# Performance work log

Hardware: AMD Instinct MI355X
Metric: run time of the kernel (lower is better)

The kernel has to match this reference:

```python
import jax, jax.numpy as jnp
import numpy as np


def median_filter(image, kernel_size):
    """kxk sliding-window median with reflect padding, same spatial size.
    image: [B, C, H, W] float. kernel_size: odd Python int."""
    k = int(kernel_size)
    p = k // 2
    B, C, H, W = image.shape
    xp = jnp.pad(image, ((0, 0), (0, 0), (p, p), (p, p)), mode='reflect')
    # k*k shifted views stacked on a new last axis: [B, C, H, W, k*k]
    windows = jnp.stack(
        [xp[:, :, i:i + H, j:j + W] for i in range(k) for j in range(k)],
        axis=-1,
    )
    # k odd -> k*k odd -> exact middle element (matches torch.median selection)
    return jnp.median(windows, axis=-1)


def setup_inputs() -> dict:
    key = jax.random.key(0)
    k1, _ = jax.random.split(key)
    image = jax.random.uniform(k1, (8, 3, 512, 512), dtype=jnp.float32)
    mask = jnp.ones((8, 1, 512, 512), dtype=jnp.float32)
    return {"image": image, "mask": mask, "kernel_size": 5}


def reference(image, mask, kernel_size):
    med = median_filter(image, kernel_size)
    # passthrough=True: (median - image).detach() + image
    out = image + jax.lax.stop_gradient(med - image)
    return (out, mask)
```

## Files before the change

kernel.cpp:

```cpp
#include <hip/hip_runtime.h>
#include <cstddef>
#include <cstdint>


#define OTW 64
#define OTH 32

using u32 = uint32_t;

__device__ __forceinline__ u32 pmin(u32 a, u32 b) {
    u32 r;
    asm("v_pk_min_f16 %0, %1, %2" : "=v"(r) : "v"(a), "v"(b));
    return r;
}
__device__ __forceinline__ u32 pmax(u32 a, u32 b) {
    u32 r;
    asm("v_pk_max_f16 %0, %1, %2" : "=v"(r) : "v"(a), "v"(b));
    return r;
}
__device__ __forceinline__ void cep(u32& a, u32& b) {
    u32 lo = pmin(a, b);
    u32 hi = pmax(a, b);
    a = lo;
    b = hi;
}

typedef __fp16 h2_t __attribute__((ext_vector_type(2)));

__device__ __forceinline__ u32 pkrtz(float a, float b) {
    h2_t v = __builtin_amdgcn_cvt_pkrtz(a, b);
    u32 u;
    __builtin_memcpy(&u, &v, 4);
    return u;
}
__device__ __forceinline__ float lo16(u32 v) {
    unsigned short s = (unsigned short)(v & 0xffffu);
    __fp16 h;
    __builtin_memcpy(&h, &s, 2);
    return (float)h;
}
__device__ __forceinline__ float hi16(u32 v) {
    unsigned short s = (unsigned short)(v >> 16);
    __fp16 h;
    __builtin_memcpy(&h, &s, 2);
    return (float)h;
}

__device__ __forceinline__ void sort5p(u32 x[5]) {
    cep(x[0], x[1]); cep(x[3], x[4]); cep(x[2], x[4]); cep(x[2], x[3]);
    cep(x[0], x[3]); cep(x[0], x[2]); cep(x[1], x[4]); cep(x[1], x[3]);
    cep(x[1], x[2]);
}

__device__ __forceinline__ void oem22p(u32 x0, u32 x1, u32 y0, u32 y1,
                                       u32 z[4]) {
    u32 d0 = pmin(x0, y0), d1 = pmax(x0, y0);
    u32 e0 = pmin(x1, y1), e1 = pmax(x1, y1);
    z[0] = d0;
    z[1] = pmin(d1, e0);
    z[2] = pmax(d1, e0);
    z[3] = e1;
}

__device__ __forceinline__ void oem33p(u32 x0, u32 x1, u32 x2, u32 y0, u32 y1,
                                       u32 y2, u32 z[6]) {
    u32 d[4];
    oem22p(x0, x2, y0, y2, d);
    u32 e0 = pmin(x1, y1);
    u32 e1 = pmax(x1, y1);
    z[0] = d[0];
    z[1] = pmin(d[1], e0); z[2] = pmax(d[1], e0);
    z[3] = pmin(d[2], e1); z[4] = pmax(d[2], e1);
    z[5] = d[3];
}

__device__ __forceinline__ void oem55p(const u32 x[5], const u32 y[5],
                                       u32 z[10]) {
    u32 d[6];
    oem33p(x[0], x[2], x[4], y[0], y[2], y[4], d);
    u32 e[4];
    oem22p(x[1], x[3], y[1], y[3], e);
    z[0] = d[0];
    z[1] = pmin(d[1], e[0]); z[2] = pmax(d[1], e[0]);
    z[3] = pmin(d[2], e[1]); z[4] = pmax(d[2], e[1]);
    z[5] = pmin(d[3], e[2]); z[6] = pmax(d[3], e[2]);
    z[7] = pmin(d[4], e[3]); z[8] = pmax(d[4], e[3]);
    z[9] = d[5];
}

__device__ __forceinline__ void oem1010_mid_p(const u32 a[10], const u32 b[10],
                                              u32 u[6]) {
    u32 ae[5] = {a[0], a[2], a[4], a[6], a[8]};
    u32 be[5] = {b[0], b[2], b[4], b[6], b[8]};
    u32 ao[5] = {a[1], a[3], a[5], a[7], a[9]};
    u32 bo[5] = {b[1], b[3], b[5], b[7], b[9]};
    u32 d[10], e[10];
    oem55p(ae, be, d);
    oem55p(ao, bo, e);
    u[0] = pmin(d[4], e[3]); u[1] = pmax(d[4], e[3]);
    u[2] = pmin(d[5], e[4]); u[3] = pmax(d[5], e[4]);
    u[4] = pmin(d[6], e[5]); u[5] = pmax(d[6], e[5]);
}

__device__ __forceinline__ u32 oem65_z5_p(const u32 u[6], const u32 v[5]) {
    u32 d[6];
    oem33p(u[0], u[2], u[4], v[0], v[2], v[4], d);
    u32 dp1 = pmax(u[1], v[1]);
    u32 t1 = pmin(dp1, u[5]);
    u32 e2 = pmax(t1, pmin(u[3], v[3]));
    return pmin(d[3], e2);
}

__device__ __forceinline__ void medrow_p(const u32 c[8][5], u32 med4[4]) {
    u32 M12[10], M34[10], M56[10];
    oem55p(c[1], c[2], M12);
    oem55p(c[3], c[4], M34);
    u32 u[6];
    oem1010_mid_p(M12, M34, u);
    med4[0] = oem65_z5_p(u, c[0]);
    med4[1] = oem65_z5_p(u, c[5]);
    oem55p(c[5], c[6], M56);
    oem1010_mid_p(M34, M56, u);
    med4[2] = oem65_z5_p(u, c[2]);
    med4[3] = oem65_z5_p(u, c[7]);
}

__device__ __forceinline__ int reflect_idx(int i, int n) {
    i = i < 0 ? -i : i;
    i = i >= n ? 2 * n - 2 - i : i;
    return i;
}

__global__ __launch_bounds__(256) void median5_kernel(
    const float* __restrict__ img, const float* __restrict__ mask,
    float* __restrict__ out, const int* __restrict__ kptr, int H, int W,
    int nimg, long img_total) {
    const int tx = threadIdx.x;
    const int ty = threadIdx.y;
    const int x0 = blockIdx.x * OTW;
    const int y0 = blockIdx.y * OTH;
    const int z = blockIdx.z;

    if (z >= nimg) {
        const size_t base = (size_t)(z - nimg) * H * W;
        const int ox = x0 + 4 * tx;
        const int oy = y0 + 2 * ty;
        const float* ms = mask + base + (size_t)oy * W + ox;
        float* md = out + img_total + base + (size_t)oy * W + ox;
        *reinterpret_cast<float4*>(md) = *reinterpret_cast<const float4*>(ms);
        *reinterpret_cast<float4*>(md + W) =
            *reinterpret_cast<const float4*>(ms + W);
        return;
    }
    if (*kptr != 5) return;

    __shared__ float tile[OTH + 4][OTW + 4 + 1];

    const float* __restrict__ src = img + (size_t)z * H * W;
    const int tid = ty * 16 + tx;

    const int NEL = (OTH + 4) * (OTW + 4);
#pragma unroll
    for (int s = 0; s < 10; ++s) {
        int idx = tid + s * 256;
        if (idx < NEL) {
            int r = idx / (OTW + 4);
            int c = idx - r * (OTW + 4);
            int gy = reflect_idx(y0 - 2 + r, H);
            int gx = reflect_idx(x0 - 2 + c, W);
            tile[r][c] = src[(size_t)gy * W + gx];
        }
    }
    __syncthreads();

    float c[8][6];
#pragma unroll
    for (int r = 0; r < 6; ++r) {
#pragma unroll
        for (int j = 0; j < 8; j += 2) {
            float2 v =
                *reinterpret_cast<const float2*>(&tile[2 * ty + r][4 * tx + j]);
            c[j][r] = v.x;
            c[j + 1][r] = v.y;
        }
    }

    u32 P[8][5];
#pragma unroll
    for (int j = 0; j < 8; ++j) {
#pragma unroll
        for (int i = 0; i < 5; ++i) P[j][i] = pkrtz(c[j][i], c[j][i + 1]);
        sort5p(P[j]);
    }

    u32 medp[4];
    medrow_p(P, medp);

    const int ox = x0 + 4 * tx;
    const int oyA = y0 + 2 * ty;
    float* dst = out + (size_t)z * H * W + (size_t)oyA * W + ox;
    *reinterpret_cast<float4*>(dst) =
        make_float4(lo16(medp[0]), lo16(medp[1]), lo16(medp[2]), lo16(medp[3]));
    *reinterpret_cast<float4*>(dst + W) =
        make_float4(hi16(medp[0]), hi16(medp[1]), hi16(medp[2]), hi16(medp[3]));
}

#define MAXK 7
__global__ void median_generic_kernel(const float* __restrict__ img,
                                      float* __restrict__ out,
                                      const int* __restrict__ kptr, int H,
                                      int W, long total) {
    const int k = *kptr;
    if (k == 5 || k > MAXK || (k & 1) == 0 || k < 1) return;
    const long stride = (long)gridDim.x * blockDim.x;
    long i0 = (long)blockIdx.x * blockDim.x + threadIdx.x;
    if (k == 1) {
        for (long i = i0; i < total; i += stride) out[i] = img[i];
        return;
    }
    const int p = k / 2;
    const int n = k * k;
    const int m = n / 2;
    float win[MAXK * MAXK];
    for (long i = i0; i < total; i += stride) {
        int x = (int)(i % W);
        long t = i / W;
        int y = (int)(t % H);
        long img_id = t / H;
        const float* src = img + img_id * (long)H * W;
        int cnt = 0;
        for (int dy = -p; dy <= p; ++dy) {
            int gy = reflect_idx(y + dy, H);
            for (int dx = -p; dx <= p; ++dx) {
                int gx = reflect_idx(x + dx, W);
                win[cnt++] = src[(long)gy * W + gx];
            }
        }
        for (int a = 0; a <= m; ++a) {
            int mi = a;
            for (int b = a + 1; b < n; ++b)
                if (win[b] < win[mi]) mi = b;
            float tv = win[a];
            win[a] = win[mi];
            win[mi] = tv;
        }
        out[i] = win[m];
    }
}

extern "C" void kernel_launch(void* const* d_in, const int* in_sizes, int n_in,
                              void* d_out, int out_size, void* d_ws,
                              size_t ws_size, hipStream_t stream) {
    const float* img = (const float*)d_in[0];
    const float* mask = (const float*)d_in[1];
    const int* kptr = (const int*)d_in[2];
    float* out = (float*)d_out;

    const int H = 512, W = 512;
    const long img_elems = in_sizes[0];
    const long mask_elems = in_sizes[1];
    const int nimg = (int)(img_elems / ((long)H * W));
    const int nmask = (int)(mask_elems / ((long)H * W));

    dim3 block(16, 16);
    dim3 grid(W / OTW, H / OTH, nimg + nmask);
    median5_kernel<<<grid, block, 0, stream>>>(img, mask, out, kptr, H, W,
                                               nimg, img_elems);

    median_generic_kernel<<<512, 256, 0, stream>>>(img, out, kptr, H, W,
                                                   img_elems);
}
```

Baseline: 28.29 us.

## Vectorize halo tile loads and fold generic median path into main kernel

The shared-memory tile load changes from scalar per-element loads with division and double reflection to float4 row loads for the interior, plus a small scalar pass that writes the four halo columns into extra slots at the end of each row. The read-back indexes those relocated halo columns for edge threads. The separate generic-k kernel launch is removed and its work moved into a noinline device function called from the main kernel, which saves one kernel launch per call. The cost is more complex indexing and a 68-wide tile without padding, which may bring back LDS bank conflicts.

```diff
diff --git a/kernel.cpp b/kernel.cpp
--- a/kernel.cpp
+++ b/kernel.cpp
@@ -131,6 +131,48 @@
     return i;
 }
 
+#define MAXK 7
+__device__ __noinline__ void generic_path(const float* __restrict__ src,
+                                          float* __restrict__ dst, int k,
+                                          int H, int W, int ox, int oy) {
+    if (k < 1 || k > MAXK || (k & 1) == 0) return;
+    if (k == 1) {
+#pragma unroll
+        for (int yy = 0; yy < 2; ++yy)
+#pragma unroll
+            for (int xx = 0; xx < 4; ++xx)
+                dst[(size_t)(oy + yy) * W + ox + xx] =
+                    src[(size_t)(oy + yy) * W + ox + xx];
+        return;
+    }
+    const int p = k / 2;
+    const int n = k * k;
+    const int m = n / 2;
+    float win[MAXK * MAXK];
+    for (int yy = 0; yy < 2; ++yy) {
+        for (int xx = 0; xx < 4; ++xx) {
+            int x = ox + xx, y = oy + yy;
+            int cnt = 0;
+            for (int dy = -p; dy <= p; ++dy) {
+                int gy = reflect_idx(y + dy, H);
+                for (int dx = -p; dx <= p; ++dx) {
+                    int gx = reflect_idx(x + dx, W);
+                    win[cnt++] = src[(size_t)gy * W + gx];
+                }
+            }
+            for (int a = 0; a <= m; ++a) {
+                int mi = a;
+                for (int b = a + 1; b < n; ++b)
+                    if (win[b] < win[mi]) mi = b;
+                float tv = win[a];
+                win[a] = win[mi];
+                win[mi] = tv;
+            }
+            dst[(size_t)y * W + x] = win[m];
+        }
+    }
+}
+
 __global__ __launch_bounds__(256) void median5_kernel(
     const float* __restrict__ img, const float* __restrict__ mask,
     float* __restrict__ out, const int* __restrict__ kptr, int H, int W,
@@ -152,37 +194,60 @@
             *reinterpret_cast<const float4*>(ms + W);
         return;
     }
-    if (*kptr != 5) return;
-
-    __shared__ float tile[OTH + 4][OTW + 4 + 1];
 
     const float* __restrict__ src = img + (size_t)z * H * W;
+    const int k = *kptr;
+    if (k != 5) {
+        generic_path(src, out + (size_t)z * H * W, k, H, W, x0 + 4 * tx,
+                     y0 + 2 * ty);
+        return;
+    }
+
+    __shared__ float tile[36][68];
+
     const int tid = ty * 16 + tx;
-
-    const int NEL = (OTH + 4) * (OTW + 4);
-#pragma unroll
-    for (int s = 0; s < 10; ++s) {
-        int idx = tid + s * 256;
-        if (idx < NEL) {
-            int r = idx / (OTW + 4);
-            int c = idx - r * (OTW + 4);
-            int gy = reflect_idx(y0 - 2 + r, H);
-            int gx = reflect_idx(x0 - 2 + c, W);
-            tile[r][c] = src[(size_t)gy * W + gx];
-        }
+    const int c4 = tid & 15;
+    const int ra = tid >> 4;
+
+#pragma unroll
+    for (int pass = 0; pass < 2; ++pass) {
+        int r = ra + 16 * pass;
+        int gy = reflect_idx(y0 - 2 + r, H);
+        float4 v = *reinterpret_cast<const float4*>(
+            &src[(size_t)gy * W + x0 + 4 * c4]);
+        *reinterpret_cast<float4*>(&tile[r][4 * c4]) = v;
+    }
+    if (tid < 64) {
+        int r = 32 + ra;
+        int gy = reflect_idx(y0 - 2 + r, H);
+        float4 v = *reinterpret_cast<const float4*>(
+            &src[(size_t)gy * W + x0 + 4 * c4]);
+        *reinterpret_cast<float4*>(&tile[r][4 * c4]) = v;
+    }
+    if (tid < 144) {
+        int r = tid >> 2;
+        int j = tid & 3;
+        int gx = reflect_idx(x0 + ((j < 2) ? (j - 2) : (62 + j)), W);
+        int gy = reflect_idx(y0 - 2 + r, H);
+        tile[r][64 + j] = src[(size_t)gy * W + gx];
     }
     __syncthreads();
 
+    const int cA = (tx == 0) ? 64 : 4 * tx - 2;
+    const int cB = 4 * tx;
+    const int cD = (tx == 15) ? 66 : 4 * tx + 4;
     float c[8][6];
 #pragma unroll
     for (int r = 0; r < 6; ++r) {
-#pragma unroll
-        for (int j = 0; j < 8; j += 2) {
-            float2 v =
-                *reinterpret_cast<const float2*>(&tile[2 * ty + r][4 * tx + j]);
-            c[j][r] = v.x;
-            c[j + 1][r] = v.y;
-        }
+        const float* row = &tile[2 * ty + r][0];
+        float2 v0 = *reinterpret_cast<const float2*>(row + cA);
+        float2 v1 = *reinterpret_cast<const float2*>(row + cB);
+        float2 v2 = *reinterpret_cast<const float2*>(row + cB + 2);
+        float2 v3 = *reinterpret_cast<const float2*>(row + cD);
+        c[0][r] = v0.x; c[1][r] = v0.y;
+        c[2][r] = v1.x; c[3][r] = v1.y;
+        c[4][r] = v2.x; c[5][r] = v2.y;
+        c[6][r] = v3.x; c[7][r] = v3.y;
     }
 
     u32 P[8][5];
@@ -205,49 +270,6 @@
         make_float4(hi16(medp[0]), hi16(medp[1]), hi16(medp[2]), hi16(medp[3]));
 }
 
-#define MAXK 7
-__global__ void median_generic_kernel(const float* __restrict__ img,
-                                      float* __restrict__ out,
-                                      const int* __restrict__ kptr, int H,
-                                      int W, long total) {
-    const int k = *kptr;
-    if (k == 5 || k > MAXK || (k & 1) == 0 || k < 1) return;
-    const long stride = (long)gridDim.x * blockDim.x;
-    long i0 = (long)blockIdx.x * blockDim.x + threadIdx.x;
-    if (k == 1) {
-        for (long i = i0; i < total; i += stride) out[i] = img[i];
-        return;
-    }
-    const int p = k / 2;
-    const int n = k * k;
-    const int m = n / 2;
-    float win[MAXK * MAXK];
-    for (long i = i0; i < total; i += stride) {
-        int x = (int)(i % W);
-        long t = i / W;
-        int y = (int)(t % H);
-        long img_id = t / H;
-        const float* src = img + img_id * (long)H * W;
-        int cnt = 0;
-        for (int dy = -p; dy <= p; ++dy) {
-            int gy = reflect_idx(y + dy, H);
-            for (int dx = -p; dx <= p; ++dx) {
-                int gx = reflect_idx(x + dx, W);
-                win[cnt++] = src[(long)gy * W + gx];
-            }
-        }
-        for (int a = 0; a <= m; ++a) {
-            int mi = a;
-            for (int b = a + 1; b < n; ++b)
-                if (win[b] < win[mi]) mi = b;
-            float tv = win[a];
-            win[a] = win[mi];
-            win[mi] = tv;
-        }
-        out[i] = win[m];
-    }
-}
-
 extern "C" void kernel_launch(void* const* d_in, const int* in_sizes, int n_in,
                               void* d_out, int out_size, void* d_ws,
                               size_t ws_size, hipStream_t stream) {
@@ -266,7 +288,4 @@
     dim3 grid(W / OTW, H / OTH, nimg + nmask);
     median5_kernel<<<grid, block, 0, stream>>>(img, mask, out, kptr, H, W,
                                                nimg, img_elems);
-
-    median_generic_kernel<<<512, 256, 0, stream>>>(img, out, kptr, H, W,
-                                                   img_elems);
-}
+}
```

Result: faster. 25.84 us (-8.6%).
